# Kernel tuning notes

Hardware: AMD Instinct MI355X
Metric: run time of the kernel (lower is better)

## Reference

```python
import jax, jax.numpy as jnp
import numpy as np
import math

EMB = 1024
HEADS = 16
B, S = 2, 2048


def setup_inputs() -> dict:
    key = jax.random.key(0)
    k_x, k_wq, k_bq, k_wu, k_bu = jax.random.split(key, 5)
    lim = 1.0 / math.sqrt(EMB)
    x = jax.random.normal(k_x, (B, S, EMB), dtype=jnp.float32)
    # nn.Linear weights: [out, in], uniform(-lim, lim)
    wq = jax.random.uniform(k_wq, (EMB, EMB), jnp.float32, -lim, lim)
    bq = jax.random.uniform(k_bq, (EMB,), jnp.float32, -lim, lim)
    wu = jax.random.uniform(k_wu, (EMB, EMB), jnp.float32, -lim, lim)
    bu = jax.random.uniform(k_bu, (EMB,), jnp.float32, -lim, lim)
    return {"x": x, "wq": wq, "bq": bq, "wu": wu, "bu": bu}


def reference(x, wq, bq, wu, bu):
    b, s, emb = x.shape
    hd = emb // HEADS
    # NOTE: faithful to the original bug — Q, K, V all come from toqueries
    q = jnp.einsum('bse,oe->bso', x, wq) + bq  # [B,S,emb]
    # faithful (buggy) reshape: heads in LEADING dim
    qh = q.reshape(HEADS, b, s, hd)
    kh = qh
    vh = qh
    scale = 1.0 / math.sqrt(emb)  # faithful: sqrt(emb), not sqrt(hd)
    scores = jnp.einsum('hbqd,hbkd->hbqk', qh, kh) * scale  # [H,B,S,S]
    attn = jax.nn.softmax(scores, axis=-1)
    out = jnp.einsum('hbqk,hbkd->hbqd', attn, vh)  # [H,B,S,hd]
    out = out.reshape(b, s, emb)
    return jnp.einsum('bse,oe->bso', out, wu) + bu
```

## Files before the change

kernel.cpp:

```cpp
#include <hip/hip_runtime.h>
#include <stdint.h>
#include <math.h>

#define EMB 1024
#define HEADS 16
#define NB 2
#define NS 2048
#define HD 64
#define NTOK (NB*NS)
#define KVBLK 64
#define SEXP2 0.04508421676368185f

typedef __attribute__((ext_vector_type(8))) short short8;
typedef __attribute__((ext_vector_type(4))) float f32x4;
typedef __attribute__((ext_vector_type(4))) unsigned int u32x4;

__device__ inline unsigned short f2bf(float f) {
  unsigned int x = __builtin_bit_cast(unsigned int, f);
  x += 0x7FFFu + ((x >> 16) & 1u);
  return (unsigned short)(x >> 16);
}

__device__ inline unsigned cvt_pk_bf16(float lo, float hi) {
  unsigned d;
  asm("v_cvt_pk_bf16_f32 %0, %1, %2" : "=v"(d) : "v"(lo), "v"(hi));
  return d;
}

__device__ inline void gld16(const void* g, void* l) {
  __builtin_amdgcn_global_load_lds(
      (const __attribute__((address_space(1))) unsigned int*)g,
      (__attribute__((address_space(3))) unsigned int*)l, 16, 0, 0);
}

__global__ void cvt_bf16x3_kernel(const float* __restrict__ s0,
                                  unsigned short* __restrict__ d0, int n0,
                                  const float* __restrict__ s1,
                                  unsigned short* __restrict__ d1, int n1,
                                  const float* __restrict__ s2,
                                  unsigned short* __restrict__ d2, int n2) {
  int i = (blockIdx.x * blockDim.x + threadIdx.x) * 8;
  const float* s; unsigned short* d;
  if (i < n0) { s = s0 + i; d = d0 + i; }
  else if (i - n0 < n1) { s = s1 + (i - n0); d = d1 + (i - n0); }
  else if (i - n0 - n1 < n2) { s = s2 + (i - n0 - n1); d = d2 + (i - n0 - n1); }
  else return;
  float4 v0 = *reinterpret_cast<const float4*>(s);
  float4 v1 = *reinterpret_cast<const float4*>(s + 4);
  short8 o;
  o[0] = (short)f2bf(v0.x); o[1] = (short)f2bf(v0.y);
  o[2] = (short)f2bf(v0.z); o[3] = (short)f2bf(v0.w);
  o[4] = (short)f2bf(v1.x); o[5] = (short)f2bf(v1.y);
  o[6] = (short)f2bf(v1.z); o[7] = (short)f2bf(v1.w);
  *reinterpret_cast<short8*>(d) = o;
}

__global__ __launch_bounds__(256) void transpose_kernel(
    const unsigned short* __restrict__ src, unsigned short* __restrict__ dst) {
  __shared__ unsigned short t[64][72];
  const int slab = blockIdx.y, kt = blockIdx.x;
  const unsigned short* s = src + ((size_t)slab * NS + kt * 64) * HD;
  unsigned short* d = dst + (size_t)slab * HD * NS + kt * 64;
  const int tid = threadIdx.x;
  #pragma unroll
  for (int c = 0; c < 2; ++c) {
    int idx = c * 256 + tid;
    int row = idx >> 3, col = (idx & 7) * 8;
    short8 v = *reinterpret_cast<const short8*>(s + row * HD + col);
    *reinterpret_cast<short8*>(&t[row][col]) = v;
  }
  __syncthreads();
  #pragma unroll
  for (int c = 0; c < 2; ++c) {
    int idx = c * 256 + tid;
    int drow = idx >> 3, col = (idx & 7) * 8;
    short8 v;
    #pragma unroll
    for (int j = 0; j < 8; ++j) {
      int p = col + j;
      int kv = (p & 32) | (((p >> 2) & 1) << 4) | (((p >> 3) & 3) << 2) | (p & 3);
      v[j] = t[kv][drow];
    }
    *reinterpret_cast<short8*>(d + (size_t)drow * NS + col) = v;
  }
}

template<bool OUT_BF16>
__global__ __launch_bounds__(256) void gemm_bt_kernel(
    const unsigned short* __restrict__ A,
    const unsigned short* __restrict__ Bw,
    const float* __restrict__ bias,
    void* __restrict__ Cout,
    float oscale,
    int M, int N, int K) {
  __shared__ __align__(16) unsigned short As[2][64 * 64];
  __shared__ __align__(16) unsigned short Bs[2][64 * 64];
  const int tid = threadIdx.x;
  const int lane = tid & 63;
  const int wave = tid >> 6;
  const int wr = wave >> 1, wc = wave & 1;
  const int g = lane >> 4, r = lane & 15;
  const int brow = blockIdx.y * 64;
  const int bcol = blockIdx.x * 64;

  const f32x4 zf = {0.f, 0.f, 0.f, 0.f};
  f32x4 acc[2][2];
  #pragma unroll
  for (int m = 0; m < 2; ++m)
    #pragma unroll
    for (int n = 0; n < 2; ++n) acc[m][n] = zf;

  auto stage = [&](int bb, int k0) {
    #pragma unroll
    for (int i = 0; i < 2; ++i) {
      int base = i * 4096 + wave * 1024;
      int L = base + lane * 16;
      int row = L >> 7, lsl = ((L >> 4) & 7) ^ (row & 7);
      gld16((const char*)A + ((size_t)(brow + row) * K + k0) * 2 + lsl * 16,
            (char*)&As[bb][0] + base);
    }
    #pragma unroll
    for (int i = 0; i < 2; ++i) {
      int base = i * 4096 + wave * 1024;
      int L = base + lane * 16;
      int row = L >> 7, lsl = ((L >> 4) & 7) ^ (row & 7);
      gld16((const char*)Bw + ((size_t)(bcol + row) * K + k0) * 2 + lsl * 16,
            (char*)&Bs[bb][0] + base);
    }
  };

  stage(0, 0);
  int cur = 0;
  for (int k0 = 0; k0 < K; k0 += 64) {
    __syncthreads();
    if (k0 + 64 < K) stage(cur ^ 1, k0 + 64);
    const char* Ac = (const char*)&As[cur][0];
    const char* Bc = (const char*)&Bs[cur][0];
    short8 af[2][2], bfr[2][2];
    #pragma unroll
    for (int m = 0; m < 2; ++m) {
      int row = wr * 32 + m * 16 + r;
      #pragma unroll
      for (int kk = 0; kk < 2; ++kk)
        af[m][kk] = *reinterpret_cast<const short8*>(
            Ac + row * 128 + ((kk * 64 + g * 16) ^ ((row & 7) << 4)));
    }
    #pragma unroll
    for (int n = 0; n < 2; ++n) {
      int row = wc * 32 + n * 16 + r;
      #pragma unroll
      for (int kk = 0; kk < 2; ++kk)
        bfr[n][kk] = *reinterpret_cast<const short8*>(
            Bc + row * 128 + ((kk * 64 + g * 16) ^ ((row & 7) << 4)));
    }
    #pragma unroll
    for (int kk = 0; kk < 2; ++kk)
      #pragma unroll
      for (int m = 0; m < 2; ++m)
        #pragma unroll
        for (int n = 0; n < 2; ++n)
          acc[m][n] = __builtin_amdgcn_mfma_f32_16x16x32_bf16(af[m][kk], bfr[n][kk], acc[m][n], 0, 0, 0);
    cur ^= 1;
  }

  #pragma unroll
  for (int n = 0; n < 2; ++n) {
    int col = bcol + wc * 32 + n * 16 + r;
    float bv = bias[col];
    #pragma unroll
    for (int m = 0; m < 2; ++m) {
      #pragma unroll
      for (int reg = 0; reg < 4; ++reg) {
        int row = brow + wr * 32 + m * 16 + g * 4 + reg;
        float v = acc[m][n][reg] + bv;
        if (OUT_BF16)
          ((unsigned short*)Cout)[(size_t)row * N + col] = f2bf(v * oscale);
        else
          ((float*)Cout)[(size_t)row * N + col] = v;
      }
    }
  }
}

__global__ __launch_bounds__(512) void attn_kernel(
    const unsigned short* __restrict__ qhb,
    const unsigned short* __restrict__ vtb,
    unsigned short* __restrict__ ob) {
  const int bid = blockIdx.x;
  const int xcd = bid & 7, idx = bid >> 3;
  const int slab = xcd * 4 + (idx >> 4);
  const int qtile = idx & 15;
  const unsigned short* Qs = qhb + (size_t)slab * NS * HD;
  const unsigned short* Vts = vtb + (size_t)slab * HD * NS;
  unsigned short* Os = ob + (size_t)slab * NS * HD;
  const int tid = threadIdx.x;
  const int lane = tid & 63;
  const int wave = tid >> 6;
  const int qsub = wave >> 1;
  const int h = wave & 1;
  const int g = lane >> 4, r = lane & 15;
  const int qrow0 = qtile * 128 + qsub * 32;
  const int rkey = (r & 7) << 4;

  __shared__ __align__(16) unsigned short K_lds[2][2][KVBLK * HD];
  __shared__ __align__(16) unsigned short Vt_lds[2][2][HD * KVBLK];

  auto stage = [&](int bb, int t) {
    int kt2 = 2 * t + h;
    const char* Kg = (const char*)Qs + (size_t)kt2 * 8192;
    const char* Vg = (const char*)Vts + (size_t)kt2 * 128;
    #pragma unroll
    for (int i = 0; i < 2; ++i) {
      int base = (qsub * 2 + i) * 1024;
      int L = base + lane * 16;
      int row = L >> 7, lsl = ((L >> 4) & 7) ^ (row & 7);
      gld16(Kg + row * 128 + lsl * 16, (char*)&K_lds[h][bb][0] + base);
      gld16(Vg + (size_t)row * (NS * 2) + lsl * 16, (char*)&Vt_lds[h][bb][0] + base);
    }
  };

  short8 aq[2][2];
  #pragma unroll
  for (int m = 0; m < 2; ++m)
    #pragma unroll
    for (int kk = 0; kk < 2; ++kk)
      aq[m][kk] = *reinterpret_cast<const short8*>(
          &Qs[(size_t)(qrow0 + m * 16 + r) * HD + kk * 32 + g * 8]);

  const f32x4 zf = {0.f, 0.f, 0.f, 0.f};
  f32x4 o_acc[2][4];
  float l_lane[2] = {0.f, 0.f};
  #pragma unroll
  for (int m = 0; m < 2; ++m)
    #pragma unroll
    for (int n = 0; n < 4; ++n) o_acc[m][n] = zf;

  stage(0, 0);
  int cur = 0;
  for (int t = 0; t < NS / KVBLK / 2; ++t) {
    __syncthreads();
    if (t + 1 < NS / KVBLK / 2) stage(cur ^ 1, t + 1);
    const char* Kc = (const char*)&K_lds[h][cur][0];
    const char* Vc = (const char*)&Vt_lds[h][cur][0];

    f32x4 s[2][4];
    __builtin_amdgcn_s_setprio(1);
    #pragma unroll
    for (int jb = 0; jb < 4; ++jb) {
      short8 bk[2];
      #pragma unroll
      for (int kk = 0; kk < 2; ++kk)
        bk[kk] = *reinterpret_cast<const short8*>(
            Kc + (jb * 16 + r) * 128 + ((kk * 64 + g * 16) ^ rkey));
      #pragma unroll
      for (int m = 0; m < 2; ++m) {
        s[m][jb] = zf;
        #pragma unroll
        for (int kk = 0; kk < 2; ++kk)
          s[m][jb] = __builtin_amdgcn_mfma_f32_16x16x32_bf16(bk[kk], aq[m][kk], s[m][jb], 0, 0, 0);
      }
    }
    __builtin_amdgcn_s_setprio(0);

    short8 ap[2][2];
    #pragma unroll
    for (int m = 0; m < 2; ++m) {
      float p[4][4];
      #pragma unroll
      for (int jb = 0; jb < 4; ++jb)
        #pragma unroll
        for (int reg = 0; reg < 4; ++reg)
          p[jb][reg] = __builtin_amdgcn_exp2f(s[m][jb][reg]);
      float t0 = (p[0][0] + p[0][1]) + (p[0][2] + p[0][3]);
      float t1 = (p[1][0] + p[1][1]) + (p[1][2] + p[1][3]);
      float t2 = (p[2][0] + p[2][1]) + (p[2][2] + p[2][3]);
      float t3 = (p[3][0] + p[3][1]) + (p[3][2] + p[3][3]);
      l_lane[m] += (t0 + t1) + (t2 + t3);
      #pragma unroll
      for (int kk = 0; kk < 2; ++kk) {
        u32x4 w;
        w.x = cvt_pk_bf16(p[2 * kk][0], p[2 * kk][1]);
        w.y = cvt_pk_bf16(p[2 * kk][2], p[2 * kk][3]);
        w.z = cvt_pk_bf16(p[2 * kk + 1][0], p[2 * kk + 1][1]);
        w.w = cvt_pk_bf16(p[2 * kk + 1][2], p[2 * kk + 1][3]);
        ap[m][kk] = __builtin_bit_cast(short8, w);
      }
    }

    __builtin_amdgcn_s_setprio(1);
    #pragma unroll
    for (int n = 0; n < 4; ++n) {
      short8 bv[2];
      #pragma unroll
      for (int kk = 0; kk < 2; ++kk)
        bv[kk] = *reinterpret_cast<const short8*>(
            Vc + (n * 16 + r) * 128 + ((kk * 64 + g * 16) ^ rkey));
      #pragma unroll
      for (int m = 0; m < 2; ++m)
        #pragma unroll
        for (int kk = 0; kk < 2; ++kk)
          o_acc[m][n] = __builtin_amdgcn_mfma_f32_16x16x32_bf16(ap[m][kk], bv[kk], o_acc[m][n], 0, 0, 0);
    }
    __builtin_amdgcn_s_setprio(0);
    cur ^= 1;
  }

  __syncthreads();
  char* redO = (char*)&K_lds[0][0][0];
  char* redL = (char*)&Vt_lds[0][0][0];
  if (h == 1) {
    #pragma unroll
    for (int m = 0; m < 2; ++m)
      #pragma unroll
      for (int n = 0; n < 4; ++n)
        *reinterpret_cast<f32x4*>(redO + qsub * 8192 + (m * 4 + n) * 1024 + lane * 16) = o_acc[m][n];
    float2 lp; lp.x = l_lane[0]; lp.y = l_lane[1];
    *reinterpret_cast<float2*>(redL + qsub * 512 + lane * 8) = lp;
  }
  __syncthreads();
  if (h == 0) {
    #pragma unroll
    for (int m = 0; m < 2; ++m)
      #pragma unroll
      for (int n = 0; n < 4; ++n)
        o_acc[m][n] += *reinterpret_cast<f32x4*>(
            redO + qsub * 8192 + (m * 4 + n) * 1024 + lane * 16);
    float2 lp = *reinterpret_cast<float2*>(redL + qsub * 512 + lane * 8);
    l_lane[0] += lp.x; l_lane[1] += lp.y;

    const float rsqc = 1.0f / sqrtf(SEXP2);
    #pragma unroll
    for (int m = 0; m < 2; ++m) {
      float l = l_lane[m];
      l += __shfl_xor(l, 16);
      l += __shfl_xor(l, 32);
      #pragma unroll
      for (int reg = 0; reg < 4; ++reg) {
        float inv = rsqc / __shfl(l, g * 4 + reg);
        int row = qrow0 + m * 16 + g * 4 + reg;
        #pragma unroll
        for (int n = 0; n < 4; ++n)
          Os[(size_t)row * HD + n * 16 + r] = f2bf(o_acc[m][n][reg] * inv);
      }
    }
  }
}

extern "C" void kernel_launch(void* const* d_in, const int* in_sizes, int n_in,
                              void* d_out, int out_size, void* d_ws, size_t ws_size,
                              hipStream_t stream) {
  const float* x  = (const float*)d_in[0];
  const float* wq = (const float*)d_in[1];
  const float* bq = (const float*)d_in[2];
  const float* wu = (const float*)d_in[3];
  const float* bu = (const float*)d_in[4];
  float* out = (float*)d_out;

  char* ws = (char*)d_ws;
  unsigned short* xb  = (unsigned short*)(ws);
  unsigned short* qhb = (unsigned short*)(ws + (8u  << 20));
  unsigned short* ob  = (unsigned short*)(ws + (16u << 20));
  unsigned short* wqb = (unsigned short*)(ws + (24u << 20));
  unsigned short* wub = (unsigned short*)(ws + (26u << 20));

  const int nx = NTOK * EMB, nw = EMB * EMB;
  cvt_bf16x3_kernel<<<((nx + 2 * nw) / 8 + 255) / 256, 256, 0, stream>>>(
      x, xb, nx, wq, wqb, nw, wu, wub, nw);

  gemm_bt_kernel<true><<<dim3(EMB / 64, NTOK / 64), 256, 0, stream>>>(
      xb, wqb, bq, qhb, sqrtf(SEXP2), NTOK, EMB, EMB);

  unsigned short* vtb = xb;
  transpose_kernel<<<dim3(NS / 64, HEADS * NB), 256, 0, stream>>>(qhb, vtb);

  attn_kernel<<<dim3(512), 512, 0, stream>>>(qhb, vtb, ob);

  gemm_bt_kernel<false><<<dim3(EMB / 64, NTOK / 64), 256, 0, stream>>>(
      ob, wub, bu, out, 1.0f, NTOK, EMB, EMB);
}
```

Before: 89.07 us.

## Split attention KV range across four waves per query group with 1024-thread blocks

Each attention block now launches 1024 threads, with four waves per 32-row query group instead of two. Each wave handles every fourth KV tile, and the partial outputs are reduced through LDS in two passes. The LDS double buffering is replaced by a single buffer that is loaded and then synchronised each iteration, which removes the overlap of loads with compute. The aim is more waves in flight to hide latency, at the cost of extra barriers, a larger reduction, and no prefetch overlap.

```diff
diff --git a/kernel.cpp b/kernel.cpp
--- a/kernel.cpp
+++ b/kernel.cpp
@@ -182,7 +182,7 @@
   }
 }
 
-__global__ __launch_bounds__(512) void attn_kernel(
+__global__ __launch_bounds__(1024, 8) void attn_kernel(
     const unsigned short* __restrict__ qhb,
     const unsigned short* __restrict__ vtb,
     unsigned short* __restrict__ ob) {
@@ -196,26 +196,27 @@
   const int tid = threadIdx.x;
   const int lane = tid & 63;
   const int wave = tid >> 6;
-  const int qsub = wave >> 1;
-  const int h = wave & 1;
+  const int qsub = wave >> 2;
+  const int h = wave & 3;
   const int g = lane >> 4, r = lane & 15;
   const int qrow0 = qtile * 128 + qsub * 32;
   const int rkey = (r & 7) << 4;
 
-  __shared__ __align__(16) unsigned short K_lds[2][2][KVBLK * HD];
-  __shared__ __align__(16) unsigned short Vt_lds[2][2][HD * KVBLK];
-
-  auto stage = [&](int bb, int t) {
-    int kt2 = 2 * t + h;
-    const char* Kg = (const char*)Qs + (size_t)kt2 * 8192;
-    const char* Vg = (const char*)Vts + (size_t)kt2 * 128;
+  __shared__ __align__(16) char smem[65536];
+  char* Kst = smem + h * 8192;
+  char* Vst = smem + 32768 + h * 8192;
+
+  auto stage = [&](int t) {
+    int kt4 = 4 * t + h;
+    const char* Kg = (const char*)Qs + (size_t)kt4 * 8192;
+    const char* Vg = (const char*)Vts + (size_t)kt4 * 128;
     #pragma unroll
     for (int i = 0; i < 2; ++i) {
       int base = (qsub * 2 + i) * 1024;
       int L = base + lane * 16;
       int row = L >> 7, lsl = ((L >> 4) & 7) ^ (row & 7);
-      gld16(Kg + row * 128 + lsl * 16, (char*)&K_lds[h][bb][0] + base);
-      gld16(Vg + (size_t)row * (NS * 2) + lsl * 16, (char*)&Vt_lds[h][bb][0] + base);
+      gld16(Kg + row * 128 + lsl * 16, Kst + base);
+      gld16(Vg + (size_t)row * (NS * 2) + lsl * 16, Vst + base);
     }
   };
 
@@ -235,13 +236,11 @@
     #pragma unroll
     for (int n = 0; n < 4; ++n) o_acc[m][n] = zf;
 
-  stage(0, 0);
-  int cur = 0;
-  for (int t = 0; t < NS / KVBLK / 2; ++t) {
+  for (int t = 0; t < 8; ++t) {
+    stage(t);
     __syncthreads();
-    if (t + 1 < NS / KVBLK / 2) stage(cur ^ 1, t + 1);
-    const char* Kc = (const char*)&K_lds[h][cur][0];
-    const char* Vc = (const char*)&Vt_lds[h][cur][0];
+    const char* Kc = Kst;
+    const char* Vc = Vst;
 
     f32x4 s[2][4];
     __builtin_amdgcn_s_setprio(1);
@@ -302,31 +301,49 @@
           o_acc[m][n] = __builtin_amdgcn_mfma_f32_16x16x32_bf16(ap[m][kk], bv[kk], o_acc[m][n], 0, 0, 0);
     }
     __builtin_amdgcn_s_setprio(0);
-    cur ^= 1;
-  }
-
-  __syncthreads();
-  char* redO = (char*)&K_lds[0][0][0];
-  char* redL = (char*)&Vt_lds[0][0][0];
-  if (h == 1) {
-    #pragma unroll
-    for (int m = 0; m < 2; ++m)
-      #pragma unroll
-      for (int n = 0; n < 4; ++n)
-        *reinterpret_cast<f32x4*>(redO + qsub * 8192 + (m * 4 + n) * 1024 + lane * 16) = o_acc[m][n];
+    __syncthreads();
+  }
+
+  char* redL = smem;
+  char* redO = smem + 8192;
+  if (h != 0) {
+    int slot = (h - 1) * 4 + qsub;
     float2 lp; lp.x = l_lane[0]; lp.y = l_lane[1];
-    *reinterpret_cast<float2*>(redL + qsub * 512 + lane * 8) = lp;
+    *reinterpret_cast<float2*>(redL + slot * 512 + lane * 8) = lp;
+    #pragma unroll
+    for (int n = 0; n < 4; ++n)
+      *reinterpret_cast<f32x4*>(redO + slot * 4096 + n * 1024 + lane * 16) = o_acc[0][n];
   }
   __syncthreads();
   if (h == 0) {
     #pragma unroll
-    for (int m = 0; m < 2; ++m)
+    for (int w = 0; w < 3; ++w) {
+      int slot = w * 4 + qsub;
+      float2 lp = *reinterpret_cast<float2*>(redL + slot * 512 + lane * 8);
+      l_lane[0] += lp.x; l_lane[1] += lp.y;
       #pragma unroll
       for (int n = 0; n < 4; ++n)
-        o_acc[m][n] += *reinterpret_cast<f32x4*>(
-            redO + qsub * 8192 + (m * 4 + n) * 1024 + lane * 16);
-    float2 lp = *reinterpret_cast<float2*>(redL + qsub * 512 + lane * 8);
-    l_lane[0] += lp.x; l_lane[1] += lp.y;
+        o_acc[0][n] += *reinterpret_cast<f32x4*>(
+            redO + slot * 4096 + n * 1024 + lane * 16);
+    }
+  }
+  __syncthreads();
+  if (h != 0) {
+    int slot = (h - 1) * 4 + qsub;
+    #pragma unroll
+    for (int n = 0; n < 4; ++n)
+      *reinterpret_cast<f32x4*>(redO + slot * 4096 + n * 1024 + lane * 16) = o_acc[1][n];
+  }
+  __syncthreads();
+  if (h == 0) {
+    #pragma unroll
+    for (int w = 0; w < 3; ++w) {
+      int slot = w * 4 + qsub;
+      #pragma unroll
+      for (int n = 0; n < 4; ++n)
+        o_acc[1][n] += *reinterpret_cast<f32x4*>(
+            redO + slot * 4096 + n * 1024 + lane * 16);
+    }
 
     const float rsqc = 1.0f / sqrtf(SEXP2);
     #pragma unroll
@@ -373,7 +390,7 @@
   unsigned short* vtb = xb;
   transpose_kernel<<<dim3(NS / 64, HEADS * NB), 256, 0, stream>>>(qhb, vtb);
 
-  attn_kernel<<<dim3(512), 512, 0, stream>>>(qhb, vtb, ob);
+  attn_kernel<<<dim3(512), 1024, 0, stream>>>(qhb, vtb, ob);
 
   gemm_bt_kernel<false><<<dim3(EMB / 64, NTOK / 64), 256, 0, stream>>>(
       ob, wub, bu, out, 1.0f, NTOK, EMB, EMB);
```

Result: slower. 341.7 us (+283.7%).

## Drop LDS double buffering in attention kernel to halve shared memory

Applied to the files above, without the earlier changes.

Replaces the double-buffered K/V LDS staging with a single buffer: each iteration loads its tile, syncs, computes, then syncs again before the next load. The end-of-kernel cross-wave reduction is split into two passes so it fits in the smaller LDS. This halves LDS per block, which could allow more resident blocks per CU. In exchange, global-load latency is no longer overlapped with MFMA compute and the kernel gains extra barriers.

```diff
diff --git a/kernel.cpp b/kernel.cpp
--- a/kernel.cpp
+++ b/kernel.cpp
@@ -202,10 +202,10 @@
   const int qrow0 = qtile * 128 + qsub * 32;
   const int rkey = (r & 7) << 4;
 
-  __shared__ __align__(16) unsigned short K_lds[2][2][KVBLK * HD];
-  __shared__ __align__(16) unsigned short Vt_lds[2][2][HD * KVBLK];
-
-  auto stage = [&](int bb, int t) {
+  __shared__ __align__(16) unsigned short K_lds[2][KVBLK * HD];
+  __shared__ __align__(16) unsigned short Vt_lds[2][HD * KVBLK];
+
+  auto stage = [&](int t) {
     int kt2 = 2 * t + h;
     const char* Kg = (const char*)Qs + (size_t)kt2 * 8192;
     const char* Vg = (const char*)Vts + (size_t)kt2 * 128;
@@ -214,8 +214,8 @@
       int base = (qsub * 2 + i) * 1024;
       int L = base + lane * 16;
       int row = L >> 7, lsl = ((L >> 4) & 7) ^ (row & 7);
-      gld16(Kg + row * 128 + lsl * 16, (char*)&K_lds[h][bb][0] + base);
-      gld16(Vg + (size_t)row * (NS * 2) + lsl * 16, (char*)&Vt_lds[h][bb][0] + base);
+      gld16(Kg + row * 128 + lsl * 16, (char*)&K_lds[h][0] + base);
+      gld16(Vg + (size_t)row * (NS * 2) + lsl * 16, (char*)&Vt_lds[h][0] + base);
     }
   };
 
@@ -235,13 +235,11 @@
     #pragma unroll
     for (int n = 0; n < 4; ++n) o_acc[m][n] = zf;
 
-  stage(0, 0);
-  int cur = 0;
-  for (int t = 0; t < NS / KVBLK / 2; ++t) {
+  for (int t = 0; t < 16; ++t) {
+    stage(t);
     __syncthreads();
-    if (t + 1 < NS / KVBLK / 2) stage(cur ^ 1, t + 1);
-    const char* Kc = (const char*)&K_lds[h][cur][0];
-    const char* Vc = (const char*)&Vt_lds[h][cur][0];
+    const char* Kc = (const char*)&K_lds[h][0];
+    const char* Vc = (const char*)&Vt_lds[h][0];
 
     f32x4 s[2][4];
     __builtin_amdgcn_s_setprio(1);
@@ -302,31 +300,39 @@
           o_acc[m][n] = __builtin_amdgcn_mfma_f32_16x16x32_bf16(ap[m][kk], bv[kk], o_acc[m][n], 0, 0, 0);
     }
     __builtin_amdgcn_s_setprio(0);
-    cur ^= 1;
-  }
-
-  __syncthreads();
-  char* redO = (char*)&K_lds[0][0][0];
-  char* redL = (char*)&Vt_lds[0][0][0];
+    __syncthreads();
+  }
+
+  char* redO = (char*)&K_lds[0][0];
+  char* redL = (char*)&Vt_lds[0][0];
   if (h == 1) {
-    #pragma unroll
-    for (int m = 0; m < 2; ++m)
-      #pragma unroll
-      for (int n = 0; n < 4; ++n)
-        *reinterpret_cast<f32x4*>(redO + qsub * 8192 + (m * 4 + n) * 1024 + lane * 16) = o_acc[m][n];
     float2 lp; lp.x = l_lane[0]; lp.y = l_lane[1];
     *reinterpret_cast<float2*>(redL + qsub * 512 + lane * 8) = lp;
+    #pragma unroll
+    for (int n = 0; n < 4; ++n)
+      *reinterpret_cast<f32x4*>(redO + qsub * 4096 + n * 1024 + lane * 16) = o_acc[0][n];
   }
   __syncthreads();
   if (h == 0) {
-    #pragma unroll
-    for (int m = 0; m < 2; ++m)
-      #pragma unroll
-      for (int n = 0; n < 4; ++n)
-        o_acc[m][n] += *reinterpret_cast<f32x4*>(
-            redO + qsub * 8192 + (m * 4 + n) * 1024 + lane * 16);
     float2 lp = *reinterpret_cast<float2*>(redL + qsub * 512 + lane * 8);
     l_lane[0] += lp.x; l_lane[1] += lp.y;
+    #pragma unroll
+    for (int n = 0; n < 4; ++n)
+      o_acc[0][n] += *reinterpret_cast<f32x4*>(
+          redO + qsub * 4096 + n * 1024 + lane * 16);
+  }
+  __syncthreads();
+  if (h == 1) {
+    #pragma unroll
+    for (int n = 0; n < 4; ++n)
+      *reinterpret_cast<f32x4*>(redO + qsub * 4096 + n * 1024 + lane * 16) = o_acc[1][n];
+  }
+  __syncthreads();
+  if (h == 0) {
+    #pragma unroll
+    for (int n = 0; n < 4; ++n)
+      o_acc[1][n] += *reinterpret_cast<f32x4*>(
+          redO + qsub * 4096 + n * 1024 + lane * 16);
 
     const float rsqc = 1.0f / sqrtf(SEXP2);
     #pragma unroll
```

After: 102.2 us. 1.15x slower.
